# Performance work log

Hardware: AMD Instinct MI355X
Metric: run time of the kernel (lower is better)

The kernel has to match this reference:

```python
import jax, jax.numpy as jnp
from jax import lax
import numpy as np

K = 3  # kernel size


def _conv_same(x, k_hwio):
    # x: [B,H,W,C], k_hwio: [K,K,C,F], stride 1, SAME padding (== TF extract_patches SAME)
    return lax.conv_general_dilated(
        x, k_hwio, window_strides=(1, 1), padding='SAME',
        dimension_numbers=('NHWC', 'HWIO', 'NHWC'))


def _maxpool2(x):
    # tf.keras MaxPooling2D(): pool 2x2, stride 2, VALID
    return lax.reduce_window(x, -jnp.inf, lax.max,
                             (1, 2, 2, 1), (1, 2, 2, 1), 'VALID')


def setup_inputs() -> dict:
    key = jax.random.key(0)
    k0, k1, k2, k3 = jax.random.split(key, 4)
    B, H, W, Cin, F = 16, 64, 64, 3, 32
    inputs = jax.random.normal(k0, (B, H, W, Cin), dtype=jnp.float32)
    W0 = jax.random.normal(k1, (K, K, Cin, F), dtype=jnp.float32) * 0.05  # conv0 HWIO
    b0 = jnp.zeros((F,), dtype=jnp.float32)
    # SharedWeights: w [filters, K*K*C] (TF patch order: ki, kj, c), b [filters]
    w = jax.random.normal(k2, (F, K * K * F), dtype=jnp.float32) * 0.01
    b = jnp.zeros((F,), dtype=jnp.float32)
    Dflat = (H // 4) * (W // 4) * F  # two 2x2 maxpools
    Wd = jax.random.normal(k3, (Dflat, 10), dtype=jnp.float32) * 0.02
    bd = jnp.zeros((10,), dtype=jnp.float32)
    return dict(inputs=inputs, W0=W0, b0=b0, w=w, b=b, Wd=Wd, bd=bd)


def reference(inputs, W0, b0, w, b, Wd, bd):
    # MyConv2D math: extract_patches (SAME) -> [B,H,W,K*K*C] with feature order
    # (ki,kj,c); then w * patches[...,None,:] summed over last axis + b.
    # That is exactly a stride-1 SAME conv with kernel w.reshape(F,K,K,C) -> HWIO.
    F, KKc = w.shape
    C = KKc // (K * K)
    k_shared = jnp.transpose(w.reshape(F, K, K, C), (1, 2, 3, 0))  # HWIO

    x = jax.nn.relu(_conv_same(inputs, W0) + b0)       # conv0 + relu
    x = jax.nn.relu(_conv_same(x, k_shared) + b)       # conv1 + relu
    x = jax.nn.relu(_conv_same(x, k_shared) + b)       # conv2 + relu
    x = _maxpool2(x)
    x = jax.nn.relu(_conv_same(x, k_shared) + b)       # conv3 + relu
    x = jax.nn.relu(_conv_same(x, k_shared) + b)       # conv4 + relu
    x = _maxpool2(x)
    x = x.reshape(x.shape[0], -1)                      # Flatten (NHWC row-major)
    logits = x @ Wd + bd                               # Dense(10)
    return jax.nn.softmax(logits, axis=-1)
```

## Files before the change

### kernel.cpp

```cpp
#include <hip/hip_runtime.h>
#include <math.h>


typedef __attribute__((ext_vector_type(8))) short bf16x8;
typedef __attribute__((ext_vector_type(4))) float f32x4;

__device__ __align__(16) unsigned short g_wbf[32 * 288];

#define A64e ((size_t)0)
#define B64e ((size_t)(16 * 66 * 66 * 32))
#define A32e ((size_t)(2 * 16 * 66 * 66 * 32))
#define B32e (A32e + (size_t)(16 * 34 * 34 * 32))
#define Dne  (B32e + (size_t)(16 * 34 * 34 * 32))

__device__ __forceinline__ unsigned short f2bf(float x) {
  union { float f; unsigned u; } v;
  v.f = x;
  return (unsigned short)((v.u + 0x7FFFu + ((v.u >> 16) & 1u)) >> 16);
}
__device__ __forceinline__ float bf2f(unsigned short x) {
  union { unsigned u; float f; } v;
  v.u = ((unsigned)x) << 16;
  return v.f;
}

__global__ __launch_bounds__(256) void conv0_prep(
    const float* __restrict__ in, const float* __restrict__ W0,
    const float* __restrict__ b0, const float* __restrict__ wsh,
    unsigned short* __restrict__ ws) {
  if (blockIdx.x >= 512) {
    int i = (blockIdx.x - 512) * 256 + threadIdx.x;
    if (i < 1152) {
      const int o0 = i * 8;
      const int f = o0 / 288;
      const int rem = o0 - f * 288;
      const int tap = rem >> 5;
      const int pos0 = rem & 31;
      const int g = pos0 >> 3;
      unsigned short u[8];
#pragma unroll
      for (int j = 0; j < 8; ++j) {
        const int c = (j < 4) ? 4 * g + j : 16 + 4 * g + (j - 4);
        u[j] = f2bf(wsh[f * 288 + tap * 32 + c]);
      }
      uint4 o;
      o.x = u[0] | ((unsigned)u[1] << 16);
      o.y = u[2] | ((unsigned)u[3] << 16);
      o.z = u[4] | ((unsigned)u[5] << 16);
      o.w = u[6] | ((unsigned)u[7] << 16);
      *(uint4*)(g_wbf + o0) = o;
      return;
    }
    i -= 1152;
    if (i >= 12544) return;
    size_t off;
    if (i < 8320) {
      const size_t base = (i < 4160) ? A64e : B64e;
      if (i >= 4160) i -= 4160;
      if (i < 2112) {
        const int b = i / 132, rem = i - b * 132;
        const int rs = rem / 66, ch = rem - rs * 66;
        off = base + (size_t)((b * 66 + (rs ? 65 : 0)) * 66) * 32 + ch * 32;
      } else {
        i -= 2112;
        const int b = i >> 7, rem = i & 127;
        const int r = rem >> 1, side = rem & 1;
        off = base + (size_t)((b * 66 + 1 + r) * 66 + (side ? 65 : 0)) * 32;
      }
    } else {
      i -= 8320;
      const size_t base = (i < 2112) ? A32e : B32e;
      if (i >= 2112) i -= 2112;
      if (i < 1088) {
        const int b = i / 68, rem = i - b * 68;
        const int rs = rem / 34, ch = rem - rs * 34;
        off = base + (size_t)((b * 34 + (rs ? 33 : 0)) * 34) * 32 + ch * 32;
      } else {
        i -= 1088;
        const int b = i >> 6, rem = i & 63;
        const int r = rem >> 1, side = rem & 1;
        off = base + (size_t)((b * 34 + 1 + r) * 34 + (side ? 33 : 0)) * 32;
      }
    }
    uint4* p = (uint4*)(ws + off);
    const uint4 z = {0u, 0u, 0u, 0u};
    p[0] = z; p[1] = z; p[2] = z; p[3] = z;
    return;
  }

  const int fg = blockIdx.x & 1;
  const int p = (blockIdx.x >> 1) * 256 + threadIdx.x;
  const int b = p >> 12, rem = p & 4095, h = rem >> 6, w = rem & 63;

  float iv[3][3][3];
#pragma unroll
  for (int r = 0; r < 3; ++r) {
    const int hh = h - 1 + r;
    const bool vr = (unsigned)hh < 64u;
#pragma unroll
    for (int j = 0; j < 3; ++j) {
      const int col = w - 1 + j;
      const bool ok = vr && ((unsigned)col < 64u);
      const float* ip = in + (((b << 6) + hh) * 64 + col) * 3;
      iv[r][j][0] = ok ? ip[0] : 0.f;
      iv[r][j][1] = ok ? ip[1] : 0.f;
      iv[r][j][2] = ok ? ip[2] : 0.f;
    }
  }

  float acc[16];
#pragma unroll
  for (int f = 0; f < 16; ++f) acc[f] = b0[fg * 16 + f];

#pragma unroll
  for (int dy = 0; dy < 3; ++dy)
#pragma unroll
    for (int dx = 0; dx < 3; ++dx)
#pragma unroll
      for (int c = 0; c < 3; ++c) {
        const float ival = iv[dy][dx][c];
        const float* wp = W0 + (((dy * 3 + dx) * 3) + c) * 32 + fg * 16;
#pragma unroll
        for (int f = 0; f < 16; ++f) acc[f] += ival * wp[f];
      }

  unsigned short* op =
      ws + A64e + ((size_t)(b * 66 + 1 + h) * 66 + 1 + w) * 32 + 4 * fg;
#pragma unroll
  for (int gp = 0; gp < 4; ++gp) {
    unsigned short u0 = f2bf(fmaxf(acc[4 * gp + 0], 0.f));
    unsigned short u1 = f2bf(fmaxf(acc[4 * gp + 1], 0.f));
    unsigned short u2 = f2bf(fmaxf(acc[4 * gp + 2], 0.f));
    unsigned short u3 = f2bf(fmaxf(acc[4 * gp + 3], 0.f));
    uint2 o;
    o.x = u0 | ((unsigned)u1 << 16);
    o.y = u2 | ((unsigned)u3 << 16);
    *(uint2*)(op + 8 * gp) = o;
  }
}

template <int LGS, bool POOL, bool OPAD>
__global__ __launch_bounds__(256, 4) void conv_mfma(
    const unsigned short* __restrict__ act, const float* __restrict__ bsh,
    unsigned short* __restrict__ outp) {
  constexpr int S = 1 << LGS, PS = S + 2, LGTC = LGS - 4, TC = S >> 4;
  const int wid = __builtin_amdgcn_readfirstlane((int)(threadIdx.x >> 6));
  const int id = blockIdx.x * 4 + wid;
  const int fhalf = id & 1;
  const int tc = (id >> 1) & (TC - 1);
  const int h2 = (id >> (1 + LGTC)) & ((S >> 1) - 1);
  const int b = id >> (LGS + LGTC);
  const int l = (int)(threadIdx.x & 63);
  const int n = l & 15, g = l >> 4;

  const unsigned short* pA = g_wbf + (fhalf * 16 + n) * 288 + 8 * g;
  bf16x8 af[9];
#pragma unroll
  for (int t = 0; t < 9; ++t) af[t] = *(const bf16x8*)(pA + t * 32);

  const unsigned short* pB =
      act + ((size_t)(b * PS + 2 * h2) * PS + tc * 16 + n) * 32 + 8 * g;
  bf16x8 bfr[4][3];
#pragma unroll
  for (int rr = 0; rr < 4; ++rr)
#pragma unroll
    for (int dx = 0; dx < 3; ++dx)
      bfr[rr][dx] = *(const bf16x8*)(pB + (rr * PS + dx) * 32);

  f32x4 acc0 = {0.f, 0.f, 0.f, 0.f};
  f32x4 acc1 = {0.f, 0.f, 0.f, 0.f};
#pragma unroll
  for (int tap = 0; tap < 9; ++tap) {
    const int dy = tap / 3, dx = tap - dy * 3;
    acc0 = __builtin_amdgcn_mfma_f32_16x16x32_bf16(af[tap], bfr[dy][dx], acc0, 0, 0, 0);
    acc1 = __builtin_amdgcn_mfma_f32_16x16x32_bf16(af[tap], bfr[dy + 1][dx], acc1, 0, 0, 0);
  }

  const float4 bias = *(const float4*)(bsh + fhalf * 16 + 4 * g);
  const float bv[4] = {bias.x, bias.y, bias.z, bias.w};
  const int opos = 8 * g + 4 * fhalf;

  if (!POOL) {
#pragma unroll
    for (int t = 0; t < 2; ++t) {
      unsigned short u[4];
#pragma unroll
      for (int r = 0; r < 4; ++r) {
        const float a = (t == 0) ? acc0[r] : acc1[r];
        u[r] = f2bf(fmaxf(a + bv[r], 0.f));
      }
      uint2 o;
      o.x = u[0] | ((unsigned)u[1] << 16);
      o.y = u[2] | ((unsigned)u[3] << 16);
      unsigned short* op = outp +
          ((size_t)(b * PS + 2 * h2 + 1 + t) * PS + 1 + tc * 16 + n) * 32 + opos;
      *(uint2*)op = o;
    }
  } else {
    float m[4];
#pragma unroll
    for (int r = 0; r < 4; ++r) {
      const float v0 = fmaxf(acc0[r] + bv[r], 0.f);
      const float v1 = fmaxf(acc1[r] + bv[r], 0.f);
      m[r] = fmaxf(v0, v1);
      m[r] = fmaxf(m[r], __shfl_xor(m[r], 1, 64));
    }
    if (!(n & 1)) {
      unsigned short u[4];
#pragma unroll
      for (int r = 0; r < 4; ++r) u[r] = f2bf(m[r]);
      uint2 o;
      o.x = u[0] | ((unsigned)u[1] << 16);
      o.y = u[2] | ((unsigned)u[3] << 16);
      unsigned short* op;
      if (OPAD) {
        op = outp + ((size_t)(b * 34 + 1 + h2) * 34 + 1 + tc * 8 + (n >> 1)) * 32 + opos;
      } else {
        op = outp + ((size_t)(b * 16 + h2) * 16 + tc * 8 + (n >> 1)) * 32 + opos;
      }
      *(uint2*)op = o;
    }
  }
}

__global__ __launch_bounds__(1024) void dense_sm(
    const unsigned short* __restrict__ x, const float* __restrict__ Wd,
    const float* __restrict__ bd, float* __restrict__ out) {
  const int b = blockIdx.x;
  const int tid = threadIdx.x;
  const unsigned short* xb = x + b * 8192;
  const int p = tid & 31, g = p >> 3, j2 = p & 7;
  const int c = (j2 < 4) ? 4 * g + j2 : 16 + 4 * g + (j2 - 4);
  const int dc = c - p;

  float acc[10];
#pragma unroll
  for (int j = 0; j < 10; ++j) acc[j] = 0.f;
#pragma unroll
  for (int it = 0; it < 8; ++it) {
    const int q = it * 1024 + tid;
    const float xv = bf2f(xb[q]);
    const float* wr = Wd + (size_t)(q + dc) * 10;
#pragma unroll
    for (int j = 0; j < 10; ++j) acc[j] += xv * wr[j];
  }
#pragma unroll
  for (int off = 32; off > 0; off >>= 1)
#pragma unroll
    for (int j = 0; j < 10; ++j) acc[j] += __shfl_down(acc[j], off, 64);

  __shared__ float red[16][10];
  const int lane = tid & 63, wv = tid >> 6;
  if (lane == 0) {
#pragma unroll
    for (int j = 0; j < 10; ++j) red[wv][j] = acc[j];
  }
  __syncthreads();
  if (tid == 0) {
    float lg[10];
    float m = -1e30f;
#pragma unroll
    for (int j = 0; j < 10; ++j) {
      float s = 0.f;
#pragma unroll
      for (int w = 0; w < 16; ++w) s += red[w][j];
      lg[j] = s + bd[j];
      m = fmaxf(m, lg[j]);
    }
    float s = 0.f;
#pragma unroll
    for (int j = 0; j < 10; ++j) {
      lg[j] = expf(lg[j] - m);
      s += lg[j];
    }
    const float inv = 1.f / s;
#pragma unroll
    for (int j = 0; j < 10; ++j) out[b * 10 + j] = lg[j] * inv;
  }
}

extern "C" void kernel_launch(void* const* d_in, const int* in_sizes, int n_in,
                              void* d_out, int out_size, void* d_ws, size_t ws_size,
                              hipStream_t stream) {
  const float* in = (const float*)d_in[0];
  const float* W0 = (const float*)d_in[1];
  const float* b0 = (const float*)d_in[2];
  const float* wsh = (const float*)d_in[3];
  const float* bsh = (const float*)d_in[4];
  const float* Wd = (const float*)d_in[5];
  const float* bd = (const float*)d_in[6];
  float* out = (float*)d_out;

  unsigned short* ws = (unsigned short*)d_ws;
  unsigned short* A64 = ws + A64e;
  unsigned short* B64 = ws + B64e;
  unsigned short* A32 = ws + A32e;
  unsigned short* B32 = ws + B32e;
  unsigned short* Dn = ws + Dne;

  conv0_prep<<<566, 256, 0, stream>>>(in, W0, b0, wsh, ws);
  conv_mfma<6, false, false><<<1024, 256, 0, stream>>>(A64, bsh, B64);
  conv_mfma<6, true, true><<<1024, 256, 0, stream>>>(B64, bsh, A32);
  conv_mfma<5, false, false><<<256, 256, 0, stream>>>(A32, bsh, B32);
  conv_mfma<5, true, false><<<256, 256, 0, stream>>>(B32, bsh, Dn);
  dense_sm<<<16, 1024, 0, stream>>>(Dn, Wd, bd, out);
}
```

Baseline: 46.10 us.

## Fuse conv3, conv4, pool, dense and softmax into one per-image LDS kernel

```diff
diff --git a/kernel.cpp b/kernel.cpp
--- a/kernel.cpp
+++ b/kernel.cpp
@@ -27,7 +27,7 @@
 __global__ __launch_bounds__(256) void conv0_prep(
     const float* __restrict__ in, const float* __restrict__ W0,
     const float* __restrict__ b0, const float* __restrict__ wsh,
-    unsigned short* __restrict__ ws) {
+    const float* __restrict__ Wd, unsigned short* __restrict__ ws) {
   if (blockIdx.x >= 512) {
     int i = (blockIdx.x - 512) * 256 + threadIdx.x;
     if (i < 1152) {
@@ -35,8 +35,7 @@
       const int f = o0 / 288;
       const int rem = o0 - f * 288;
       const int tap = rem >> 5;
-      const int pos0 = rem & 31;
-      const int g = pos0 >> 3;
+      const int g = (rem & 31) >> 3;
       unsigned short u[8];
 #pragma unroll
       for (int j = 0; j < 8; ++j) {
@@ -52,39 +51,46 @@
       return;
     }
     i -= 1152;
-    if (i >= 12544) return;
-    size_t off;
-    if (i < 8320) {
-      const size_t base = (i < 4160) ? A64e : B64e;
-      if (i >= 4160) i -= 4160;
-      if (i < 2112) {
-        const int b = i / 132, rem = i - b * 132;
-        const int rs = rem / 66, ch = rem - rs * 66;
-        off = base + (size_t)((b * 66 + (rs ? 65 : 0)) * 66) * 32 + ch * 32;
+    if (i < 12544) {
+      size_t off;
+      if (i < 8320) {
+        const size_t base = (i < 4160) ? A64e : B64e;
+        if (i >= 4160) i -= 4160;
+        if (i < 2112) {
+          const int b = i / 132, rem = i - b * 132;
+          const int rs = rem / 66, ch = rem - rs * 66;
+          off = base + (size_t)((b * 66 + (rs ? 65 : 0)) * 66) * 32 + ch * 32;
+        } else {
+          i -= 2112;
+          const int b = i >> 7, rem = i & 127;
+          const int r = rem >> 1, side = rem & 1;
+          off = base + (size_t)((b * 66 + 1 + r) * 66 + (side ? 65 : 0)) * 32;
+        }
       } else {
-        i -= 2112;
-        const int b = i >> 7, rem = i & 127;
-        const int r = rem >> 1, side = rem & 1;
-        off = base + (size_t)((b * 66 + 1 + r) * 66 + (side ? 65 : 0)) * 32;
+        i -= 8320;
+        const size_t base = (i < 2112) ? A32e : B32e;
+        if (i >= 2112) i -= 2112;
+        if (i < 1088) {
+          const int b = i / 68, rem = i - b * 68;
+          const int rs = rem / 34, ch = rem - rs * 34;
+          off = base + (size_t)((b * 34 + (rs ? 33 : 0)) * 34) * 32 + ch * 32;
+        } else {
+          i -= 1088;
+          const int b = i >> 6, rem = i & 63;
+          const int r = rem >> 1, side = rem & 1;
+          off = base + (size_t)((b * 34 + 1 + r) * 34 + (side ? 33 : 0)) * 32;
+        }
       }
-    } else {
-      i -= 8320;
-      const size_t base = (i < 2112) ? A32e : B32e;
-      if (i >= 2112) i -= 2112;
-      if (i < 1088) {
-        const int b = i / 68, rem = i - b * 68;
-        const int rs = rem / 34, ch = rem - rs * 34;
-        off = base + (size_t)((b * 34 + (rs ? 33 : 0)) * 34) * 32 + ch * 32;
-      } else {
-        i -= 1088;
-        const int b = i >> 6, rem = i & 63;
-        const int r = rem >> 1, side = rem & 1;
-        off = base + (size_t)((b * 34 + 1 + r) * 34 + (side ? 33 : 0)) * 32;
-      }
-    }
-    uint4* p = (uint4*)(ws + off);
-    const uint4 z = {0u, 0u, 0u, 0u};
-    p[0] = z; p[1] = z; p[2] = z; p[3] = z;
+      uint4* p = (uint4*)(ws + off);
+      const uint4 z = {0u, 0u, 0u, 0u};
+      p[0] = z; p[1] = z; p[2] = z; p[3] = z;
+      return;
+    }
+    i -= 12544;
+    if (i < 81920) {
+      const int j = i >> 13, q = i & 8191;
+      ws[Dne + i] = f2bf(Wd[q * 10 + j]);
+    }
     return;
   }
 
@@ -212,26 +218,126 @@
       uint2 o;
       o.x = u[0] | ((unsigned)u[1] << 16);
       o.y = u[2] | ((unsigned)u[3] << 16);
-      unsigned short* op;
-      if (OPAD) {
-        op = outp + ((size_t)(b * 34 + 1 + h2) * 34 + 1 + tc * 8 + (n >> 1)) * 32 + opos;
-      } else {
-        op = outp + ((size_t)(b * 16 + h2) * 16 + tc * 8 + (n >> 1)) * 32 + opos;
-      }
+      unsigned short* op =
+          outp + ((size_t)(b * 34 + 1 + h2) * 34 + 1 + tc * 8 + (n >> 1)) * 32 + opos;
       *(uint2*)op = o;
     }
   }
 }
 
-__global__ __launch_bounds__(1024) void dense_sm(
-    const unsigned short* __restrict__ x, const float* __restrict__ Wd,
-    const float* __restrict__ bd, float* __restrict__ out) {
+__global__ __launch_bounds__(1024) void tail(
+    const unsigned short* __restrict__ A32, const float* __restrict__ bsh,
+    const unsigned short* __restrict__ wdt, const float* __restrict__ bd,
+    float* __restrict__ out) {
+  extern __shared__ unsigned short lds[];
+  unsigned short* t3 = lds;
+  unsigned short* dn = lds + 36992;
+  float* red = (float*)(lds + 36992 + 8192);
+
   const int b = blockIdx.x;
   const int tid = threadIdx.x;
-  const unsigned short* xb = x + b * 8192;
-  const int p = tid & 31, g = p >> 3, j2 = p & 7;
-  const int c = (j2 < 4) ? 4 * g + j2 : 16 + 4 * g + (j2 - 4);
-  const int dc = c - p;
+  const int wid = __builtin_amdgcn_readfirstlane(tid >> 6);
+  const int l = tid & 63;
+  const int n = l & 15, g = l >> 4;
+  const int fhalf = wid & 1;
+
+  const unsigned short* pA = g_wbf + (fhalf * 16 + n) * 288 + 8 * g;
+  bf16x8 af[9];
+#pragma unroll
+  for (int t = 0; t < 9; ++t) af[t] = *(const bf16x8*)(pA + t * 32);
+
+  const float4 bias = *(const float4*)(bsh + fhalf * 16 + 4 * g);
+  const float bv[4] = {bias.x, bias.y, bias.z, bias.w};
+  const int opos = 8 * g + 4 * fhalf;
+
+  if (tid < 528) {
+    const int c = tid >> 2, chunk = tid & 3;
+    int row, px;
+    if (c < 68) { row = (c >= 34) ? 33 : 0; px = (c >= 34) ? c - 34 : c; }
+    else { const int c2 = c - 68; row = 1 + (c2 >> 1); px = (c2 & 1) ? 33 : 0; }
+    uint4* p = (uint4*)(t3 + ((row * 4 + chunk) * 34 + px) * 8);
+    const uint4 z = {0u, 0u, 0u, 0u};
+    *p = z;
+  }
+  __syncthreads();
+
+#pragma unroll
+  for (int u = 0; u < 4; ++u) {
+    const int idx = ((wid >> 1) << 2) + u;
+    const int h2 = idx >> 1, tc = idx & 1;
+    const unsigned short* pB =
+        A32 + ((size_t)(b * 34 + 2 * h2) * 34 + tc * 16 + n) * 32 + 8 * g;
+    bf16x8 bfr[4][3];
+#pragma unroll
+    for (int rr = 0; rr < 4; ++rr)
+#pragma unroll
+      for (int dx = 0; dx < 3; ++dx)
+        bfr[rr][dx] = *(const bf16x8*)(pB + (rr * 34 + dx) * 32);
+
+    f32x4 acc0 = {0.f, 0.f, 0.f, 0.f};
+    f32x4 acc1 = {0.f, 0.f, 0.f, 0.f};
+#pragma unroll
+    for (int tap = 0; tap < 9; ++tap) {
+      const int dy = tap / 3, dx = tap - dy * 3;
+      acc0 = __builtin_amdgcn_mfma_f32_16x16x32_bf16(af[tap], bfr[dy][dx], acc0, 0, 0, 0);
+      acc1 = __builtin_amdgcn_mfma_f32_16x16x32_bf16(af[tap], bfr[dy + 1][dx], acc1, 0, 0, 0);
+    }
+#pragma unroll
+    for (int t = 0; t < 2; ++t) {
+      unsigned short uu[4];
+#pragma unroll
+      for (int r = 0; r < 4; ++r) {
+        const float a = (t == 0) ? acc0[r] : acc1[r];
+        uu[r] = f2bf(fmaxf(a + bv[r], 0.f));
+      }
+      uint2 o;
+      o.x = uu[0] | ((unsigned)uu[1] << 16);
+      o.y = uu[2] | ((unsigned)uu[3] << 16);
+      *(uint2*)(t3 + (((2 * h2 + 1 + t) * 4 + g) * 34 + 1 + tc * 16 + n) * 8 +
+                4 * fhalf) = o;
+    }
+  }
+  __syncthreads();
+
+#pragma unroll
+  for (int u = 0; u < 4; ++u) {
+    const int idx = ((wid >> 1) << 2) + u;
+    const int h2 = idx >> 1, tc = idx & 1;
+    bf16x8 bfr[4][3];
+#pragma unroll
+    for (int rr = 0; rr < 4; ++rr)
+#pragma unroll
+      for (int dx = 0; dx < 3; ++dx)
+        bfr[rr][dx] = *(const bf16x8*)(
+            t3 + (((2 * h2 + rr) * 4 + g) * 34 + tc * 16 + n + dx) * 8);
+
+    f32x4 acc0 = {0.f, 0.f, 0.f, 0.f};
+    f32x4 acc1 = {0.f, 0.f, 0.f, 0.f};
+#pragma unroll
+    for (int tap = 0; tap < 9; ++tap) {
+      const int dy = tap / 3, dx = tap - dy * 3;
+      acc0 = __builtin_amdgcn_mfma_f32_16x16x32_bf16(af[tap], bfr[dy][dx], acc0, 0, 0, 0);
+      acc1 = __builtin_amdgcn_mfma_f32_16x16x32_bf16(af[tap], bfr[dy + 1][dx], acc1, 0, 0, 0);
+    }
+    float m[4];
+#pragma unroll
+    for (int r = 0; r < 4; ++r) {
+      const float v0 = fmaxf(acc0[r] + bv[r], 0.f);
+      const float v1 = fmaxf(acc1[r] + bv[r], 0.f);
+      m[r] = fmaxf(v0, v1);
+      m[r] = fmaxf(m[r], __shfl_xor(m[r], 1, 64));
+    }
+    if (!(n & 1)) {
+      unsigned short uu[4];
+#pragma unroll
+      for (int r = 0; r < 4; ++r) uu[r] = f2bf(m[r]);
+      uint2 o;
+      o.x = uu[0] | ((unsigned)uu[1] << 16);
+      o.y = uu[2] | ((unsigned)uu[3] << 16);
+      *(uint2*)(dn + ((h2 * 16) + tc * 8 + (n >> 1)) * 32 + fhalf * 16 + 4 * g) = o;
+    }
+  }
+  __syncthreads();
 
   float acc[10];
 #pragma unroll
@@ -239,38 +345,34 @@
 #pragma unroll
   for (int it = 0; it < 8; ++it) {
     const int q = it * 1024 + tid;
-    const float xv = bf2f(xb[q]);
-    const float* wr = Wd + (size_t)(q + dc) * 10;
-#pragma unroll
-    for (int j = 0; j < 10; ++j) acc[j] += xv * wr[j];
+    const float xv = bf2f(dn[q]);
+#pragma unroll
+    for (int j = 0; j < 10; ++j) acc[j] += xv * bf2f(wdt[j * 8192 + q]);
   }
 #pragma unroll
   for (int off = 32; off > 0; off >>= 1)
 #pragma unroll
     for (int j = 0; j < 10; ++j) acc[j] += __shfl_down(acc[j], off, 64);
-
-  __shared__ float red[16][10];
-  const int lane = tid & 63, wv = tid >> 6;
-  if (lane == 0) {
-#pragma unroll
-    for (int j = 0; j < 10; ++j) red[wv][j] = acc[j];
+  if (l == 0) {
+#pragma unroll
+    for (int j = 0; j < 10; ++j) red[wid * 10 + j] = acc[j];
   }
   __syncthreads();
   if (tid == 0) {
     float lg[10];
-    float m = -1e30f;
+    float mx = -1e30f;
 #pragma unroll
     for (int j = 0; j < 10; ++j) {
       float s = 0.f;
 #pragma unroll
-      for (int w = 0; w < 16; ++w) s += red[w][j];
+      for (int w = 0; w < 16; ++w) s += red[w * 10 + j];
       lg[j] = s + bd[j];
-      m = fmaxf(m, lg[j]);
+      mx = fmaxf(mx, lg[j]);
     }
     float s = 0.f;
 #pragma unroll
     for (int j = 0; j < 10; ++j) {
-      lg[j] = expf(lg[j] - m);
+      lg[j] = expf(lg[j] - mx);
       s += lg[j];
     }
     const float inv = 1.f / s;
@@ -295,13 +397,18 @@
   unsigned short* A64 = ws + A64e;
   unsigned short* B64 = ws + B64e;
   unsigned short* A32 = ws + A32e;
-  unsigned short* B32 = ws + B32e;
-  unsigned short* Dn = ws + Dne;
-
-  conv0_prep<<<566, 256, 0, stream>>>(in, W0, b0, wsh, ws);
+  unsigned short* WdT = ws + Dne;
+
+  const int tail_lds = (36992 + 8192) * 2 + 16 * 10 * 4;
+  static bool attr_set = false;
+  if (!attr_set) {
+    hipFuncSetAttribute((const void*)tail,
+                        hipFuncAttributeMaxDynamicSharedMemorySize, tail_lds);
+    attr_set = true;
+  }
+
+  conv0_prep<<<886, 256, 0, stream>>>(in, W0, b0, wsh, Wd, ws);
   conv_mfma<6, false, false><<<1024, 256, 0, stream>>>(A64, bsh, B64);
   conv_mfma<6, true, true><<<1024, 256, 0, stream>>>(B64, bsh, A32);
-  conv_mfma<5, false, false><<<256, 256, 0, stream>>>(A32, bsh, B32);
-  conv_mfma<5, true, false><<<256, 256, 0, stream>>>(B32, bsh, Dn);
-  dense_sm<<<16, 1024, 0, stream>>>(Dn, Wd, bd, out);
-}
+  tail<<<16, 1024, tail_lds, stream>>>(A32, bsh, WdT, bd, out);
+}
```

New measurement: 54.59 us. 18.4% more time.
